# Performance work log

Measured on AMD Instinct MI355X. Metric: run time of the kernel, lower is better.

The kernel has to match this reference:

```python
import jax, jax.numpy as jnp
import numpy as np

B, DIM, H, W = 2, 128, 64, 64
DH, HEADS, K = 32, 4, 7  # dim_head, num_heads = dim // dim_head, kernel_size


def _ln(x, g, b):
    mu = jnp.mean(x, -1, keepdims=True)
    var = jnp.mean((x - mu) ** 2, -1, keepdims=True)
    return (x - mu) * jax.lax.rsqrt(var + 1e-5) * g + b


def _na2d(x, qkv_w, qkv_b, rpb, proj_w, proj_b):
    # NATTEN-style 2D neighborhood attention, dilation=1, edge-clamped windows.
    Bb, Hh, Ww, C = x.shape
    k = K
    qkv = (x @ qkv_w.T + qkv_b).reshape(Bb, Hh, Ww, 3, HEADS, DH).transpose(3, 0, 4, 1, 2, 5)
    q = qkv[0] * (DH ** -0.5)  # [B, heads, H, W, dh]
    kt, vt = qkv[1], qkv[2]
    def starts(n):
        return jnp.clip(jnp.arange(n) - k // 2, 0, n - k)
    nh = starts(Hh)[:, None] + jnp.arange(k)  # [H, k] absolute neighbor rows
    nw = starts(Ww)[:, None] + jnp.arange(k)  # [W, k] absolute neighbor cols
    ih = nh[:, None, :, None]  # [H,1,k,1]
    iw = nw[None, :, None, :]  # [1,W,1,k]
    Kw = kt[:, :, ih, iw, :]   # [B, heads, H, W, k, k, dh]
    Vw = vt[:, :, ih, iw, :]
    attn = jnp.einsum('bnhwd,bnhwijd->bnhwij', q, Kw)  # [B,heads,H,W,k,k]
    # relative positional bias, indices in [0, 2k-2]
    bih = (nh - jnp.arange(Hh)[:, None] + (k - 1))[:, None, :, None]
    biw = (nw - jnp.arange(Ww)[:, None] + (k - 1))[None, :, None, :]
    attn = attn + rpb[:, bih, biw][None]
    attn = jax.nn.softmax(attn.reshape(Bb, HEADS, Hh, Ww, k * k), -1).reshape(Bb, HEADS, Hh, Ww, k, k)
    out = jnp.einsum('bnhwij,bnhwijd->bnhwd', attn, Vw)
    out = out.transpose(0, 2, 3, 1, 4).reshape(Bb, Hh, Ww, C)
    return out @ proj_w.T + proj_b


def setup_inputs() -> dict:
    key = jax.random.key(0)
    ks = jax.random.split(key, 8)
    d = DIM
    w = lambda k_, sh: jax.random.normal(k_, sh, jnp.float32) * 0.02
    inp = {'x': jax.random.normal(ks[0], (B, DIM, H, W), jnp.float32)}
    inp.update(g1=jnp.ones(d), be1=jnp.zeros(d), g2=jnp.ones(d), be2=jnp.zeros(d),
               g3=jnp.ones(d), be3=jnp.zeros(d), g4=jnp.ones(d), be4=jnp.zeros(d))
    inp['qkv_w'] = w(ks[1], (3 * d, d)); inp['qkv_b'] = jnp.zeros(3 * d)
    inp['rpb'] = w(ks[2], (HEADS, 2 * K - 1, 2 * K - 1))
    inp['proj_w'] = w(ks[3], (d, d)); inp['proj_b'] = jnp.zeros(d)
    inp['w1'] = w(ks[4], (d, d)); inp['bl1'] = jnp.zeros(d)
    inp['w2'] = w(ks[5], (d, d)); inp['bl2'] = jnp.zeros(d)
    inp['w3'] = w(ks[6], (d, d)); inp['bl3'] = jnp.zeros(d)
    return inp


def reference(x, g1, be1, g2, be2, g3, be3, g4, be4, qkv_w, qkv_b, rpb, proj_w, proj_b, w1, bl1, w2, bl2, w3, bl3):
    x = x.transpose(0, 2, 3, 1)  # NCHW -> NHWC
    r = x
    y = _ln(x, g1, be1)
    y = _na2d(y, qkv_w, qkv_b, rpb, proj_w, proj_b)
    y = _ln(y, g2, be2)
    y = y @ w1.T + bl1
    x = y + r
    r = x
    y = _ln(x, g3, be3)
    y = y @ w2.T + bl2
    y = jax.nn.relu(y)
    y = _ln(y, g4, be4)
    y = y @ w3.T + bl3
    x = y + r
    return x.transpose(0, 3, 1, 2)  # NHWC -> NCHW
```

## Files before the change

kernel.cpp:

```cpp
#include <hip/hip_runtime.h>
#include <hip/hip_bf16.h>
#include <cstdint>

typedef short bf16x8 __attribute__((ext_vector_type(8)));
typedef float f32x4 __attribute__((ext_vector_type(4)));

#define NTOK 8192
#define QSCALE 0.17677669529663687f

__device__ inline float b2f(short s) {
  return __uint_as_float(((unsigned)(unsigned short)s) << 16);
}
__device__ inline short f2bs(float x) {
  __hip_bfloat16 b = __float2bfloat16(x);
  return *reinterpret_cast<short*>(&b);
}
__device__ inline bf16x8 ld8(const short* p) {
  short4 lo = *reinterpret_cast<const short4*>(p);
  short4 hi = *reinterpret_cast<const short4*>(p + 4);
  bf16x8 r;
  r[0] = lo.x; r[1] = lo.y; r[2] = lo.z; r[3] = lo.w;
  r[4] = hi.x; r[5] = hi.y; r[6] = hi.z; r[7] = hi.w;
  return r;
}

__global__ __launch_bounds__(256) void k_convw(
    const float* __restrict__ qw, const float* __restrict__ pw,
    const float* __restrict__ w1, const float* __restrict__ w2,
    const float* __restrict__ w3, __hip_bfloat16* __restrict__ dst) {
  int i = blockIdx.x * 256 + threadIdx.x;
  float v;
  if (i < 49152) v = qw[i];
  else if (i < 65536) v = pw[i - 49152];
  else if (i < 81920) v = w1[i - 65536];
  else if (i < 98304) v = w2[i - 81920];
  else if (i < 114688) v = w3[i - 98304];
  else return;
  dst[i] = __float2bfloat16(v);
}

__global__ __launch_bounds__(256) void k_qkvln(
    const float* __restrict__ x, const float* __restrict__ g,
    const float* __restrict__ be, const float* __restrict__ qkv_b,
    const __hip_bfloat16* __restrict__ wqkv, float* __restrict__ r,
    __hip_bfloat16* __restrict__ qkvb) {
  __shared__ float xt[128][33];
  __shared__ __hip_bfloat16 at[32][136];
  int t = threadIdx.x;
  int m0 = blockIdx.x * 32;
  int b = m0 >> 12;
  int p0 = m0 & 4095;
  const float* xb = x + (size_t)b * 524288;
  int tw = t & 31, th = t >> 5;
#pragma unroll
  for (int i = 0; i < 16; ++i) {
    int c = i * 8 + th;
    xt[c][tw] = xb[c * 4096 + p0 + tw];
  }
  __syncthreads();
  int wid = t >> 6, lane = t & 63;
  float gg0 = g[lane], gg1 = g[lane + 64];
  float bb0 = be[lane], bb1 = be[lane + 64];
#pragma unroll
  for (int it = 0; it < 8; ++it) {
    int tt = wid * 8 + it;
    float v0 = xt[lane][tt], v1 = xt[lane + 64][tt];
    float s = v0 + v1, sq = v0 * v0 + v1 * v1;
#pragma unroll
    for (int off = 32; off; off >>= 1) {
      s += __shfl_xor(s, off);
      sq += __shfl_xor(sq, off);
    }
    float mu = s * (1.f / 128.f);
    float var = sq * (1.f / 128.f) - mu * mu;
    float rs = rsqrtf(var + 1e-5f);
    r[(size_t)(m0 + tt) * 128 + lane] = v0;
    r[(size_t)(m0 + tt) * 128 + 64 + lane] = v1;
    at[tt][lane] = __float2bfloat16((v0 - mu) * rs * gg0 + bb0);
    at[tt][lane + 64] = __float2bfloat16((v1 - mu) * rs * gg1 + bb1);
  }
  __syncthreads();
  int mw = wid >> 1, nw = wid & 1;
  int lr = lane & 15, kg = lane >> 4;
  bf16x8 af[4];
#pragma unroll
  for (int ks = 0; ks < 4; ++ks)
    af[ks] = *reinterpret_cast<const bf16x8*>(&at[mw * 16 + lr][ks * 32 + kg * 8]);
  f32x4 acc[12];
#pragma unroll
  for (int nf = 0; nf < 12; ++nf) acc[nf] = f32x4{0, 0, 0, 0};
#pragma unroll
  for (int nf = 0; nf < 12; ++nf) {
    int o = nw * 192 + nf * 16 + lr;
    const __hip_bfloat16* wp = wqkv + o * 128 + kg * 8;
#pragma unroll
    for (int ks = 0; ks < 4; ++ks) {
      bf16x8 bfr = *reinterpret_cast<const bf16x8*>(wp + ks * 32);
      acc[nf] = __builtin_amdgcn_mfma_f32_16x16x32_bf16(af[ks], bfr, acc[nf], 0, 0, 0);
    }
  }
#pragma unroll
  for (int nf = 0; nf < 12; ++nf) {
    int o = nw * 192 + nf * 16 + lr;
    float bv = qkv_b[o];
    float qs = (o < 128) ? QSCALE : 1.f;
#pragma unroll
    for (int rr = 0; rr < 4; ++rr) {
      int m = m0 + mw * 16 + kg * 4 + rr;
      qkvb[(size_t)m * 384 + o] = __float2bfloat16((acc[nf][rr] + bv) * qs);
    }
  }
}

#define NB 98
#define KP 132
#define VP 108
#define PP 132
__global__ __launch_bounds__(256) void k_attn3(
    const __hip_bfloat16* __restrict__ qkv, const float* __restrict__ rpb,
    __hip_bfloat16* __restrict__ ao) {
  __shared__ __align__(16) short smem[104 * KP + 128 * VP + 4 * 8 * PP];
  short* Kl = smem;
  short* Vt = smem + 104 * KP;
  short* Pl = Vt + 128 * VP;
  const short* qs = (const short*)qkv;
  int tid = threadIdx.x;
  int m0 = blockIdx.x * 8;
  int b = m0 >> 12, hq = (m0 >> 6) & 63, c0 = m0 & 63;
  int hs = min(max(hq - 3, 0), 57);
  int cs0 = min(max(c0 - 3, 0), 50);
#pragma unroll
  for (int it = 0; it < 7; ++it) {
    int idx = it * 256 + tid;
    if (idx < NB * 16) {
      int row = idx >> 4, sub = idx & 15;
      int rh = row / 14, rc = row - rh * 14;
      int tr = b * 4096 + (hs + rh) * 64 + min(cs0 + rc, 63);
      const short* src = qs + (size_t)tr * 384 + 128 + sub * 8;
      *(short4*)(Kl + row * KP + sub * 8) = *(const short4*)src;
      *(short4*)(Kl + row * KP + sub * 8 + 4) = *(const short4*)(src + 4);
      const short* sv = qs + (size_t)tr * 384 + 256 + sub * 8;
      short4 vlo = *(const short4*)sv;
      short4 vhi = *(const short4*)(sv + 4);
      int d0 = sub * 8;
      Vt[(d0 + 0) * VP + row] = vlo.x;
      Vt[(d0 + 1) * VP + row] = vlo.y;
      Vt[(d0 + 2) * VP + row] = vlo.z;
      Vt[(d0 + 3) * VP + row] = vlo.w;
      Vt[(d0 + 4) * VP + row] = vhi.x;
      Vt[(d0 + 5) * VP + row] = vhi.y;
      Vt[(d0 + 6) * VP + row] = vhi.z;
      Vt[(d0 + 7) * VP + row] = vhi.w;
    }
  }
  {
    int row = tid >> 1, half = tid & 1;
#pragma unroll
    for (int e = 0; e < 5; ++e) Vt[row * VP + NB + half * 5 + e] = 0;
  }
  __syncthreads();
  int h = tid >> 6, lane = tid & 63;
  int lr = lane & 15, kg = lane >> 4;
  int qrow = min(m0 + lr, NTOK - 1);
  bf16x8 aq = *reinterpret_cast<const bf16x8*>(qs + (size_t)qrow * 384 + h * 32 + kg * 8);
  f32x4 sc[7];
#pragma unroll
  for (int nt = 0; nt < 7; ++nt) {
    bf16x8 bk = ld8(Kl + (nt * 16 + lr) * KP + h * 32 + kg * 8);
    sc[nt] = __builtin_amdgcn_mfma_f32_16x16x32_bf16(aq, bk, f32x4{0, 0, 0, 0}, 0, 0, 0);
  }
  int offv[4], cmt[4];
#pragma unroll
  for (int rr = 0; rr < 4; ++rr) {
    int ct = c0 + kg * 4 + rr;
    int ws0 = min(max(ct - 3, 0), 57);
    offv[rr] = ws0 - cs0;
    cmt[rr] = cs0 + 6 - ct;
  }
  float mx[4] = {-3e38f, -3e38f, -3e38f, -3e38f};
#pragma unroll
  for (int nt = 0; nt < 7; ++nt) {
    int nbr = nt * 16 + lr;
    int rh = nbr / 14, rc = nbr - rh * 14;
    bool vn = nbr < NB;
    int ribase = h * 169 + (hs - hq + 6 + rh) * 13 + rc;
#pragma unroll
    for (int rr = 0; rr < 4; ++rr) {
      float v = -1e30f;
      if (vn && (unsigned)(rc - offv[rr]) < 7u) v = sc[nt][rr] + rpb[ribase + cmt[rr]];
      sc[nt][rr] = v;
      mx[rr] = fmaxf(mx[rr], v);
    }
  }
#pragma unroll
  for (int rr = 0; rr < 4; ++rr) {
    mx[rr] = fmaxf(mx[rr], __shfl_xor(mx[rr], 1));
    mx[rr] = fmaxf(mx[rr], __shfl_xor(mx[rr], 2));
    mx[rr] = fmaxf(mx[rr], __shfl_xor(mx[rr], 4));
    mx[rr] = fmaxf(mx[rr], __shfl_xor(mx[rr], 8));
  }
  float sum[4] = {0.f, 0.f, 0.f, 0.f};
#pragma unroll
  for (int nt = 0; nt < 7; ++nt)
#pragma unroll
    for (int rr = 0; rr < 4; ++rr) {
      float e = __expf(sc[nt][rr] - mx[rr]);
      sc[nt][rr] = e;
      sum[rr] += e;
    }
#pragma unroll
  for (int rr = 0; rr < 4; ++rr) {
    sum[rr] += __shfl_xor(sum[rr], 1);
    sum[rr] += __shfl_xor(sum[rr], 2);
    sum[rr] += __shfl_xor(sum[rr], 4);
    sum[rr] += __shfl_xor(sum[rr], 8);
  }
  short* Ph = Pl + h * 8 * PP;
  if (kg < 2) {
#pragma unroll
    for (int rr = 0; rr < 4; ++rr) {
      float inv = 1.f / sum[rr];
      int tok = kg * 4 + rr;
#pragma unroll
      for (int nt = 0; nt < 7; ++nt)
        Ph[tok * PP + nt * 16 + lr] = f2bs(sc[nt][rr] * inv);
      Ph[tok * PP + 112 + lr] = 0;
      Ph[tok * PP + 128 + (lr & 3)] = 0;
    }
  }
  __syncthreads();
  f32x4 o[2] = {f32x4{0, 0, 0, 0}, f32x4{0, 0, 0, 0}};
#pragma unroll
  for (int kt = 0; kt < 4; ++kt) {
    bf16x8 ap = ld8(Ph + (lr & 7) * PP + kt * 32 + kg * 8);
#pragma unroll
    for (int dt = 0; dt < 2; ++dt) {
      bf16x8 bv = ld8(Vt + (h * 32 + dt * 16 + lr) * VP + kt * 32 + kg * 8);
      o[dt] = __builtin_amdgcn_mfma_f32_16x16x32_bf16(ap, bv, o[dt], 0, 0, 0);
    }
  }
  if (kg < 2) {
#pragma unroll
    for (int dt = 0; dt < 2; ++dt)
#pragma unroll
      for (int rr = 0; rr < 4; ++rr) {
        int tok = kg * 4 + rr;
        ao[(size_t)(m0 + tok) * 128 + h * 32 + dt * 16 + lr] =
            __float2bfloat16(o[dt][rr]);
      }
  }
}

template <bool A_GLOBAL>
__device__ inline void gemm_stage(const __hip_bfloat16* __restrict__ Aglob,
                                  const __hip_bfloat16 (*abuf)[136],
                                  const __hip_bfloat16* __restrict__ W,
                                  int mw, int nw, int lr, int kg, f32x4 acc[4]) {
  bf16x8 af[4];
  if constexpr (A_GLOBAL) {
#pragma unroll
    for (int ks = 0; ks < 4; ++ks)
      af[ks] = *reinterpret_cast<const bf16x8*>(Aglob + (mw * 16 + lr) * 128 + ks * 32 + kg * 8);
  } else {
#pragma unroll
    for (int ks = 0; ks < 4; ++ks)
      af[ks] = *reinterpret_cast<const bf16x8*>(&abuf[mw * 16 + lr][ks * 32 + kg * 8]);
  }
#pragma unroll
  for (int nf = 0; nf < 4; ++nf) {
    int o = nw * 64 + nf * 16 + lr;
    const __hip_bfloat16* wp = W + o * 128 + kg * 8;
    acc[nf] = f32x4{0, 0, 0, 0};
#pragma unroll
    for (int ks = 0; ks < 4; ++ks) {
      bf16x8 bfr = *reinterpret_cast<const bf16x8*>(wp + ks * 32);
      acc[nf] = __builtin_amdgcn_mfma_f32_16x16x32_bf16(af[ks], bfr, acc[nf], 0, 0, 0);
    }
  }
}

__device__ inline void ln_store(f32x4 acc[4], __hip_bfloat16 (*abuf)[136],
                                float2 (*red)[2][16],
                                const float* __restrict__ g,
                                const float* __restrict__ be,
                                int mw, int nw, int lr, int kg) {
  float ps[4] = {0.f, 0.f, 0.f, 0.f}, pq[4] = {0.f, 0.f, 0.f, 0.f};
#pragma unroll
  for (int nf = 0; nf < 4; ++nf)
#pragma unroll
    for (int rr = 0; rr < 4; ++rr) {
      float v = acc[nf][rr];
      ps[rr] += v;
      pq[rr] += v * v;
    }
#pragma unroll
  for (int rr = 0; rr < 4; ++rr)
#pragma unroll
    for (int off = 1; off < 16; off <<= 1) {
      ps[rr] += __shfl_xor(ps[rr], off);
      pq[rr] += __shfl_xor(pq[rr], off);
    }
  if (lr == 0)
#pragma unroll
    for (int rr = 0; rr < 4; ++rr)
      red[mw][nw][kg * 4 + rr] = make_float2(ps[rr], pq[rr]);
  __syncthreads();
  float mu[4], rs[4];
#pragma unroll
  for (int rr = 0; rr < 4; ++rr) {
    float2 a0 = red[mw][0][kg * 4 + rr], a1 = red[mw][1][kg * 4 + rr];
    mu[rr] = (a0.x + a1.x) * (1.f / 128.f);
    float var = (a0.y + a1.y) * (1.f / 128.f) - mu[rr] * mu[rr];
    rs[rr] = rsqrtf(var + 1e-5f);
  }
#pragma unroll
  for (int nf = 0; nf < 4; ++nf) {
    int o = nw * 64 + nf * 16 + lr;
    float gv = g[o], bev = be[o];
#pragma unroll
    for (int rr = 0; rr < 4; ++rr)
      abuf[mw * 16 + kg * 4 + rr][o] =
          __float2bfloat16((acc[nf][rr] - mu[rr]) * rs[rr] * gv + bev);
  }
}

__global__ __launch_bounds__(256) void k_tail(
    const __hip_bfloat16* __restrict__ ao, const float* __restrict__ r,
    const __hip_bfloat16* __restrict__ wproj, const float* __restrict__ bproj,
    const float* __restrict__ g2, const float* __restrict__ be2,
    const __hip_bfloat16* __restrict__ w1, const float* __restrict__ b1,
    const float* __restrict__ g3, const float* __restrict__ be3,
    const __hip_bfloat16* __restrict__ w2, const float* __restrict__ b2,
    const float* __restrict__ g4, const float* __restrict__ be4,
    const __hip_bfloat16* __restrict__ w3, const float* __restrict__ b3,
    float* __restrict__ out) {
  __shared__ __hip_bfloat16 abuf[32][136];
  __shared__ float2 red[2][2][16];
  int t = threadIdx.x, wid = t >> 6, lane = t & 63;
  int mw = wid >> 1, nw = wid & 1;
  int lr = lane & 15, kg = lane >> 4;
  int m0 = blockIdx.x * 32;
  f32x4 acc[4];
  float x2f[4][4];

  gemm_stage<true>(ao + (size_t)m0 * 128, nullptr, wproj, mw, nw, lr, kg, acc);
#pragma unroll
  for (int nf = 0; nf < 4; ++nf) {
    float bv = bproj[nw * 64 + nf * 16 + lr];
#pragma unroll
    for (int rr = 0; rr < 4; ++rr) acc[nf][rr] += bv;
  }
  ln_store(acc, abuf, red, g2, be2, mw, nw, lr, kg);
  __syncthreads();

  gemm_stage<false>(nullptr, abuf, w1, mw, nw, lr, kg, acc);
#pragma unroll
  for (int nf = 0; nf < 4; ++nf) {
    int o = nw * 64 + nf * 16 + lr;
    float bv = b1[o];
#pragma unroll
    for (int rr = 0; rr < 4; ++rr) {
      int m = m0 + mw * 16 + kg * 4 + rr;
      float v = acc[nf][rr] + bv + r[(size_t)m * 128 + o];
      x2f[nf][rr] = v;
      acc[nf][rr] = v;
    }
  }
  ln_store(acc, abuf, red, g3, be3, mw, nw, lr, kg);
  __syncthreads();

  gemm_stage<false>(nullptr, abuf, w2, mw, nw, lr, kg, acc);
#pragma unroll
  for (int nf = 0; nf < 4; ++nf) {
    float bv = b2[nw * 64 + nf * 16 + lr];
#pragma unroll
    for (int rr = 0; rr < 4; ++rr) acc[nf][rr] = fmaxf(acc[nf][rr] + bv, 0.f);
  }
  ln_store(acc, abuf, red, g4, be4, mw, nw, lr, kg);
  __syncthreads();

  gemm_stage<false>(nullptr, abuf, w3, mw, nw, lr, kg, acc);
#pragma unroll
  for (int nf = 0; nf < 4; ++nf) {
    int o = nw * 64 + nf * 16 + lr;
    float bv = b3[o];
#pragma unroll
    for (int rr = 0; rr < 4; ++rr) {
      int m = m0 + mw * 16 + kg * 4 + rr;
      float v = acc[nf][rr] + bv + x2f[nf][rr];
      int bb = m >> 12, hw = m & 4095;
      out[(size_t)bb * 524288 + o * 4096 + hw] = v;
    }
  }
}

extern "C" void kernel_launch(void* const* d_in, const int* in_sizes, int n_in,
                              void* d_out, int out_size, void* d_ws,
                              size_t ws_size, hipStream_t stream) {
  const float* x = (const float*)d_in[0];
  const float* g1 = (const float*)d_in[1];
  const float* be1 = (const float*)d_in[2];
  const float* g2 = (const float*)d_in[3];
  const float* be2 = (const float*)d_in[4];
  const float* g3 = (const float*)d_in[5];
  const float* be3 = (const float*)d_in[6];
  const float* g4 = (const float*)d_in[7];
  const float* be4 = (const float*)d_in[8];
  const float* qkv_w = (const float*)d_in[9];
  const float* qkv_b = (const float*)d_in[10];
  const float* rpb = (const float*)d_in[11];
  const float* proj_w = (const float*)d_in[12];
  const float* proj_b = (const float*)d_in[13];
  const float* w1 = (const float*)d_in[14];
  const float* bl1 = (const float*)d_in[15];
  const float* w2 = (const float*)d_in[16];
  const float* bl2 = (const float*)d_in[17];
  const float* w3 = (const float*)d_in[18];
  const float* bl3 = (const float*)d_in[19];

  char* ws = (char*)d_ws;
  __hip_bfloat16* wb = (__hip_bfloat16*)ws;
  __hip_bfloat16* wb_qkv = wb;
  __hip_bfloat16* wb_proj = wb + 49152;
  __hip_bfloat16* wb_w1 = wb + 65536;
  __hip_bfloat16* wb_w2 = wb + 81920;
  __hip_bfloat16* wb_w3 = wb + 98304;
  float* r = (float*)(ws + 262144);
  __hip_bfloat16* qkvb = (__hip_bfloat16*)(ws + 4456448);
  __hip_bfloat16* ao = (__hip_bfloat16*)(ws + 10747904);

  k_convw<<<448, 256, 0, stream>>>(qkv_w, proj_w, w1, w2, w3, wb);
  k_qkvln<<<256, 256, 0, stream>>>(x, g1, be1, qkv_b, wb_qkv, r, qkvb);
  k_attn3<<<1024, 256, 0, stream>>>(qkvb, rpb, ao);
  k_tail<<<256, 256, 0, stream>>>(ao, r, wb_proj, proj_b, g2, be2, wb_w1, bl1,
                                  g3, be3, wb_w2, bl2, g4, be4, wb_w3, bl3,
                                  (float*)d_out);
}
```

Before: 56.12 us.

## Fuse attention with MLP tail and fold weight conversion into QKV kernel

Merges the weight-conversion kernel into the QKV/LayerNorm kernel, which now converts QKV weights to bf16 in registers and has each block convert a slice of the remaining weights. The attention kernel and the projection/MLP tail are fused so each block computes attention for 32 tokens in four 8-token passes and keeps the result in LDS. This removes two launches and the global round-trip of the attention output. In exchange, the attention phase runs on a quarter as many blocks with serialized passes, which reduces parallelism and latency hiding.

After: 63.38 us. +12.9%, slower.

```diff
diff --git a/kernel.cpp b/kernel.cpp
--- a/kernel.cpp
+++ b/kernel.cpp
@@ -23,30 +23,32 @@
   r[4] = hi.x; r[5] = hi.y; r[6] = hi.z; r[7] = hi.w;
   return r;
 }
-
-__global__ __launch_bounds__(256) void k_convw(
-    const float* __restrict__ qw, const float* __restrict__ pw,
-    const float* __restrict__ w1, const float* __restrict__ w2,
-    const float* __restrict__ w3, __hip_bfloat16* __restrict__ dst) {
-  int i = blockIdx.x * 256 + threadIdx.x;
-  float v;
-  if (i < 49152) v = qw[i];
-  else if (i < 65536) v = pw[i - 49152];
-  else if (i < 81920) v = w1[i - 65536];
-  else if (i < 98304) v = w2[i - 81920];
-  else if (i < 114688) v = w3[i - 98304];
-  else return;
-  dst[i] = __float2bfloat16(v);
-}
-
-__global__ __launch_bounds__(256) void k_qkvln(
+__device__ inline bf16x8 cvt8(float4 a, float4 c) {
+  bf16x8 r;
+  r[0] = f2bs(a.x); r[1] = f2bs(a.y); r[2] = f2bs(a.z); r[3] = f2bs(a.w);
+  r[4] = f2bs(c.x); r[5] = f2bs(c.y); r[6] = f2bs(c.z); r[7] = f2bs(c.w);
+  return r;
+}
+
+__global__ __launch_bounds__(256) void k_qkvcw(
     const float* __restrict__ x, const float* __restrict__ g,
     const float* __restrict__ be, const float* __restrict__ qkv_b,
-    const __hip_bfloat16* __restrict__ wqkv, float* __restrict__ r,
-    __hip_bfloat16* __restrict__ qkvb) {
+    const float* __restrict__ qkv_w, const float* __restrict__ pw,
+    const float* __restrict__ w1f, const float* __restrict__ w2f,
+    const float* __restrict__ w3f, __hip_bfloat16* __restrict__ wb,
+    float* __restrict__ r, __hip_bfloat16* __restrict__ qkvb) {
   __shared__ float xt[128][33];
   __shared__ __hip_bfloat16 at[32][136];
   int t = threadIdx.x;
+  {
+    int ci = blockIdx.x * 256 + t;
+    float cv;
+    if (ci < 16384) cv = pw[ci];
+    else if (ci < 32768) cv = w1f[ci - 16384];
+    else if (ci < 49152) cv = w2f[ci - 32768];
+    else cv = w3f[ci - 49152];
+    wb[ci] = __float2bfloat16(cv);
+  }
   int m0 = blockIdx.x * 32;
   int b = m0 >> 12;
   int p0 = m0 & 4095;
@@ -92,11 +94,13 @@
 #pragma unroll
   for (int nf = 0; nf < 12; ++nf) {
     int o = nw * 192 + nf * 16 + lr;
-    const __hip_bfloat16* wp = wqkv + o * 128 + kg * 8;
+    const float* wp = qkv_w + o * 128 + kg * 8;
 #pragma unroll
     for (int ks = 0; ks < 4; ++ks) {
-      bf16x8 bfr = *reinterpret_cast<const bf16x8*>(wp + ks * 32);
-      acc[nf] = __builtin_amdgcn_mfma_f32_16x16x32_bf16(af[ks], bfr, acc[nf], 0, 0, 0);
+      float4 wa = *reinterpret_cast<const float4*>(wp + ks * 32);
+      float4 wc = *reinterpret_cast<const float4*>(wp + ks * 32 + 4);
+      acc[nf] = __builtin_amdgcn_mfma_f32_16x16x32_bf16(af[ks], cvt8(wa, wc),
+                                                        acc[nf], 0, 0, 0);
     }
   }
 #pragma unroll
@@ -116,244 +120,235 @@
 #define KP 132
 #define VP 108
 #define PP 132
-__global__ __launch_bounds__(256) void k_attn3(
-    const __hip_bfloat16* __restrict__ qkv, const float* __restrict__ rpb,
-    __hip_bfloat16* __restrict__ ao) {
+__global__ __launch_bounds__(256) void k_fuse2(
+    const __hip_bfloat16* __restrict__ qkvb, const float* __restrict__ rpb,
+    const float* __restrict__ r, const __hip_bfloat16* __restrict__ wb,
+    const float* __restrict__ bproj,
+    const float* __restrict__ g2, const float* __restrict__ be2,
+    const float* __restrict__ b1,
+    const float* __restrict__ g3, const float* __restrict__ be3,
+    const float* __restrict__ b2,
+    const float* __restrict__ g4, const float* __restrict__ be4,
+    const float* __restrict__ b3, float* __restrict__ out) {
   __shared__ __align__(16) short smem[104 * KP + 128 * VP + 4 * 8 * PP];
+  __shared__ __align__(16) __hip_bfloat16 abuf[32][136];
+  __shared__ float2 red[2][2][16];
   short* Kl = smem;
   short* Vt = smem + 104 * KP;
   short* Pl = Vt + 128 * VP;
-  const short* qs = (const short*)qkv;
+  const short* qs = (const short*)qkvb;
   int tid = threadIdx.x;
-  int m0 = blockIdx.x * 8;
-  int b = m0 >> 12, hq = (m0 >> 6) & 63, c0 = m0 & 63;
+  int m0 = blockIdx.x * 32;
+  int b = m0 >> 12, hq = (m0 >> 6) & 63;
   int hs = min(max(hq - 3, 0), 57);
-  int cs0 = min(max(c0 - 3, 0), 50);
-#pragma unroll
-  for (int it = 0; it < 7; ++it) {
-    int idx = it * 256 + tid;
-    if (idx < NB * 16) {
-      int row = idx >> 4, sub = idx & 15;
-      int rh = row / 14, rc = row - rh * 14;
-      int tr = b * 4096 + (hs + rh) * 64 + min(cs0 + rc, 63);
-      const short* src = qs + (size_t)tr * 384 + 128 + sub * 8;
-      *(short4*)(Kl + row * KP + sub * 8) = *(const short4*)src;
-      *(short4*)(Kl + row * KP + sub * 8 + 4) = *(const short4*)(src + 4);
-      const short* sv = qs + (size_t)tr * 384 + 256 + sub * 8;
-      short4 vlo = *(const short4*)sv;
-      short4 vhi = *(const short4*)(sv + 4);
-      int d0 = sub * 8;
-      Vt[(d0 + 0) * VP + row] = vlo.x;
-      Vt[(d0 + 1) * VP + row] = vlo.y;
-      Vt[(d0 + 2) * VP + row] = vlo.z;
-      Vt[(d0 + 3) * VP + row] = vlo.w;
-      Vt[(d0 + 4) * VP + row] = vhi.x;
-      Vt[(d0 + 5) * VP + row] = vhi.y;
-      Vt[(d0 + 6) * VP + row] = vhi.z;
-      Vt[(d0 + 7) * VP + row] = vhi.w;
-    }
-  }
-  {
-    int row = tid >> 1, half = tid & 1;
-#pragma unroll
-    for (int e = 0; e < 5; ++e) Vt[row * VP + NB + half * 5 + e] = 0;
-  }
-  __syncthreads();
   int h = tid >> 6, lane = tid & 63;
   int lr = lane & 15, kg = lane >> 4;
-  int qrow = min(m0 + lr, NTOK - 1);
-  bf16x8 aq = *reinterpret_cast<const bf16x8*>(qs + (size_t)qrow * 384 + h * 32 + kg * 8);
-  f32x4 sc[7];
-#pragma unroll
-  for (int nt = 0; nt < 7; ++nt) {
-    bf16x8 bk = ld8(Kl + (nt * 16 + lr) * KP + h * 32 + kg * 8);
-    sc[nt] = __builtin_amdgcn_mfma_f32_16x16x32_bf16(aq, bk, f32x4{0, 0, 0, 0}, 0, 0, 0);
-  }
-  int offv[4], cmt[4];
-#pragma unroll
-  for (int rr = 0; rr < 4; ++rr) {
-    int ct = c0 + kg * 4 + rr;
-    int ws0 = min(max(ct - 3, 0), 57);
-    offv[rr] = ws0 - cs0;
-    cmt[rr] = cs0 + 6 - ct;
-  }
-  float mx[4] = {-3e38f, -3e38f, -3e38f, -3e38f};
-#pragma unroll
-  for (int nt = 0; nt < 7; ++nt) {
-    int nbr = nt * 16 + lr;
-    int rh = nbr / 14, rc = nbr - rh * 14;
-    bool vn = nbr < NB;
-    int ribase = h * 169 + (hs - hq + 6 + rh) * 13 + rc;
-#pragma unroll
-    for (int rr = 0; rr < 4; ++rr) {
-      float v = -1e30f;
-      if (vn && (unsigned)(rc - offv[rr]) < 7u) v = sc[nt][rr] + rpb[ribase + cmt[rr]];
-      sc[nt][rr] = v;
-      mx[rr] = fmaxf(mx[rr], v);
-    }
-  }
-#pragma unroll
-  for (int rr = 0; rr < 4; ++rr) {
-    mx[rr] = fmaxf(mx[rr], __shfl_xor(mx[rr], 1));
-    mx[rr] = fmaxf(mx[rr], __shfl_xor(mx[rr], 2));
-    mx[rr] = fmaxf(mx[rr], __shfl_xor(mx[rr], 4));
-    mx[rr] = fmaxf(mx[rr], __shfl_xor(mx[rr], 8));
-  }
-  float sum[4] = {0.f, 0.f, 0.f, 0.f};
-#pragma unroll
-  for (int nt = 0; nt < 7; ++nt)
-#pragma unroll
-    for (int rr = 0; rr < 4; ++rr) {
-      float e = __expf(sc[nt][rr] - mx[rr]);
-      sc[nt][rr] = e;
-      sum[rr] += e;
-    }
-#pragma unroll
-  for (int rr = 0; rr < 4; ++rr) {
-    sum[rr] += __shfl_xor(sum[rr], 1);
-    sum[rr] += __shfl_xor(sum[rr], 2);
-    sum[rr] += __shfl_xor(sum[rr], 4);
-    sum[rr] += __shfl_xor(sum[rr], 8);
-  }
-  short* Ph = Pl + h * 8 * PP;
-  if (kg < 2) {
-#pragma unroll
-    for (int rr = 0; rr < 4; ++rr) {
-      float inv = 1.f / sum[rr];
-      int tok = kg * 4 + rr;
-#pragma unroll
-      for (int nt = 0; nt < 7; ++nt)
-        Ph[tok * PP + nt * 16 + lr] = f2bs(sc[nt][rr] * inv);
-      Ph[tok * PP + 112 + lr] = 0;
-      Ph[tok * PP + 128 + (lr & 3)] = 0;
-    }
-  }
-  __syncthreads();
-  f32x4 o[2] = {f32x4{0, 0, 0, 0}, f32x4{0, 0, 0, 0}};
-#pragma unroll
-  for (int kt = 0; kt < 4; ++kt) {
-    bf16x8 ap = ld8(Ph + (lr & 7) * PP + kt * 32 + kg * 8);
-#pragma unroll
-    for (int dt = 0; dt < 2; ++dt) {
-      bf16x8 bv = ld8(Vt + (h * 32 + dt * 16 + lr) * VP + kt * 32 + kg * 8);
-      o[dt] = __builtin_amdgcn_mfma_f32_16x16x32_bf16(ap, bv, o[dt], 0, 0, 0);
-    }
-  }
-  if (kg < 2) {
-#pragma unroll
-    for (int dt = 0; dt < 2; ++dt)
+  const __hip_bfloat16* wproj = wb;
+  const __hip_bfloat16* w1 = wb + 16384;
+  const __hip_bfloat16* w2 = wb + 32768;
+  const __hip_bfloat16* w3 = wb + 49152;
+
+  {
+    int rowz = tid >> 1, halfz = tid & 1;
+#pragma unroll
+    for (int e = 0; e < 5; ++e) Vt[rowz * VP + NB + halfz * 5 + e] = 0;
+  }
+
+  for (int s = 0; s < 4; ++s) {
+    __syncthreads();
+    int ms = m0 + s * 8;
+    int c0s = (m0 & 63) + s * 8;
+    int cs0 = min(max(c0s - 3, 0), 50);
+#pragma unroll
+    for (int it = 0; it < 7; ++it) {
+      int idx = it * 256 + tid;
+      if (idx < NB * 16) {
+        int row = idx >> 4, sub = idx & 15;
+        int rh = row / 14, rc = row - rh * 14;
+        int tr = b * 4096 + (hs + rh) * 64 + min(cs0 + rc, 63);
+        const short* src = qs + (size_t)tr * 384 + 128 + sub * 8;
+        *(short4*)(Kl + row * KP + sub * 8) = *(const short4*)src;
+        *(short4*)(Kl + row * KP + sub * 8 + 4) = *(const short4*)(src + 4);
+        const short* sv = qs + (size_t)tr * 384 + 256 + sub * 8;
+        short4 vlo = *(const short4*)sv;
+        short4 vhi = *(const short4*)(sv + 4);
+        int d0 = sub * 8;
+        Vt[(d0 + 0) * VP + row] = vlo.x;
+        Vt[(d0 + 1) * VP + row] = vlo.y;
+        Vt[(d0 + 2) * VP + row] = vlo.z;
+        Vt[(d0 + 3) * VP + row] = vlo.w;
+        Vt[(d0 + 4) * VP + row] = vhi.x;
+        Vt[(d0 + 5) * VP + row] = vhi.y;
+        Vt[(d0 + 6) * VP + row] = vhi.z;
+        Vt[(d0 + 7) * VP + row] = vhi.w;
+      }
+    }
+    __syncthreads();
+    int qrow = min(ms + lr, NTOK - 1);
+    bf16x8 aq = *reinterpret_cast<const bf16x8*>(qs + (size_t)qrow * 384 + h * 32 + kg * 8);
+    f32x4 sc[7];
+#pragma unroll
+    for (int nt = 0; nt < 7; ++nt) {
+      bf16x8 bk = ld8(Kl + (nt * 16 + lr) * KP + h * 32 + kg * 8);
+      sc[nt] = __builtin_amdgcn_mfma_f32_16x16x32_bf16(aq, bk, f32x4{0, 0, 0, 0}, 0, 0, 0);
+    }
+    int offv[4], cmt[4];
+#pragma unroll
+    for (int rr = 0; rr < 4; ++rr) {
+      int ct = c0s + kg * 4 + rr;
+      int ws0 = min(max(ct - 3, 0), 57);
+      offv[rr] = ws0 - cs0;
+      cmt[rr] = cs0 + 6 - ct;
+    }
+    float mx[4] = {-3e38f, -3e38f, -3e38f, -3e38f};
+#pragma unroll
+    for (int nt = 0; nt < 7; ++nt) {
+      int nbr = nt * 16 + lr;
+      int rh = nbr / 14, rc = nbr - rh * 14;
+      bool vn = nbr < NB;
+      int ribase = h * 169 + (hs - hq + 6 + rh) * 13 + rc;
 #pragma unroll
       for (int rr = 0; rr < 4; ++rr) {
+        float v = -1e30f;
+        if (vn && (unsigned)(rc - offv[rr]) < 7u) v = sc[nt][rr] + rpb[ribase + cmt[rr]];
+        sc[nt][rr] = v;
+        mx[rr] = fmaxf(mx[rr], v);
+      }
+    }
+#pragma unroll
+    for (int rr = 0; rr < 4; ++rr) {
+      mx[rr] = fmaxf(mx[rr], __shfl_xor(mx[rr], 1));
+      mx[rr] = fmaxf(mx[rr], __shfl_xor(mx[rr], 2));
+      mx[rr] = fmaxf(mx[rr], __shfl_xor(mx[rr], 4));
+      mx[rr] = fmaxf(mx[rr], __shfl_xor(mx[rr], 8));
+    }
+    float sum[4] = {0.f, 0.f, 0.f, 0.f};
+#pragma unroll
+    for (int nt = 0; nt < 7; ++nt)
+#pragma unroll
+      for (int rr = 0; rr < 4; ++rr) {
+        float e = __expf(sc[nt][rr] - mx[rr]);
+        sc[nt][rr] = e;
+        sum[rr] += e;
+      }
+#pragma unroll
+    for (int rr = 0; rr < 4; ++rr) {
+      sum[rr] += __shfl_xor(sum[rr], 1);
+      sum[rr] += __shfl_xor(sum[rr], 2);
+      sum[rr] += __shfl_xor(sum[rr], 4);
+      sum[rr] += __shfl_xor(sum[rr], 8);
+    }
+    short* Ph = Pl + h * 8 * PP;
+    if (kg < 2) {
+#pragma unroll
+      for (int rr = 0; rr < 4; ++rr) {
+        float inv = 1.f / sum[rr];
         int tok = kg * 4 + rr;
-        ao[(size_t)(m0 + tok) * 128 + h * 32 + dt * 16 + lr] =
-            __float2bfloat16(o[dt][rr]);
-      }
-  }
-}
-
-template <bool A_GLOBAL>
-__device__ inline void gemm_stage(const __hip_bfloat16* __restrict__ Aglob,
-                                  const __hip_bfloat16 (*abuf)[136],
-                                  const __hip_bfloat16* __restrict__ W,
-                                  int mw, int nw, int lr, int kg, f32x4 acc[4]) {
-  bf16x8 af[4];
-  if constexpr (A_GLOBAL) {
-#pragma unroll
-    for (int ks = 0; ks < 4; ++ks)
-      af[ks] = *reinterpret_cast<const bf16x8*>(Aglob + (mw * 16 + lr) * 128 + ks * 32 + kg * 8);
-  } else {
+#pragma unroll
+        for (int nt = 0; nt < 7; ++nt)
+          Ph[tok * PP + nt * 16 + lr] = f2bs(sc[nt][rr] * inv);
+        Ph[tok * PP + 112 + lr] = 0;
+        Ph[tok * PP + 128 + (lr & 3)] = 0;
+      }
+    }
+    __syncthreads();
+    f32x4 o2[2] = {f32x4{0, 0, 0, 0}, f32x4{0, 0, 0, 0}};
+#pragma unroll
+    for (int kt = 0; kt < 4; ++kt) {
+      bf16x8 ap = ld8(Ph + (lr & 7) * PP + kt * 32 + kg * 8);
+#pragma unroll
+      for (int dt = 0; dt < 2; ++dt) {
+        bf16x8 bv = ld8(Vt + (h * 32 + dt * 16 + lr) * VP + kt * 32 + kg * 8);
+        o2[dt] = __builtin_amdgcn_mfma_f32_16x16x32_bf16(ap, bv, o2[dt], 0, 0, 0);
+      }
+    }
+    if (kg < 2) {
+#pragma unroll
+      for (int dt = 0; dt < 2; ++dt)
+#pragma unroll
+        for (int rr = 0; rr < 4; ++rr)
+          abuf[s * 8 + kg * 4 + rr][h * 32 + dt * 16 + lr] =
+              __float2bfloat16(o2[dt][rr]);
+    }
+  }
+  __syncthreads();
+
+  int wid = tid >> 6;
+  int mw = wid >> 1, nw = wid & 1;
+  f32x4 acc[4];
+  float x2f[4][4];
+
+  auto gemm_lds = [&](const __hip_bfloat16* W) {
+    bf16x8 af[4];
 #pragma unroll
     for (int ks = 0; ks < 4; ++ks)
       af[ks] = *reinterpret_cast<const bf16x8*>(&abuf[mw * 16 + lr][ks * 32 + kg * 8]);
-  }
-#pragma unroll
-  for (int nf = 0; nf < 4; ++nf) {
-    int o = nw * 64 + nf * 16 + lr;
-    const __hip_bfloat16* wp = W + o * 128 + kg * 8;
-    acc[nf] = f32x4{0, 0, 0, 0};
-#pragma unroll
-    for (int ks = 0; ks < 4; ++ks) {
-      bf16x8 bfr = *reinterpret_cast<const bf16x8*>(wp + ks * 32);
-      acc[nf] = __builtin_amdgcn_mfma_f32_16x16x32_bf16(af[ks], bfr, acc[nf], 0, 0, 0);
-    }
-  }
-}
-
-__device__ inline void ln_store(f32x4 acc[4], __hip_bfloat16 (*abuf)[136],
-                                float2 (*red)[2][16],
-                                const float* __restrict__ g,
-                                const float* __restrict__ be,
-                                int mw, int nw, int lr, int kg) {
-  float ps[4] = {0.f, 0.f, 0.f, 0.f}, pq[4] = {0.f, 0.f, 0.f, 0.f};
-#pragma unroll
-  for (int nf = 0; nf < 4; ++nf)
-#pragma unroll
-    for (int rr = 0; rr < 4; ++rr) {
-      float v = acc[nf][rr];
-      ps[rr] += v;
-      pq[rr] += v * v;
-    }
-#pragma unroll
-  for (int rr = 0; rr < 4; ++rr)
-#pragma unroll
-    for (int off = 1; off < 16; off <<= 1) {
-      ps[rr] += __shfl_xor(ps[rr], off);
-      pq[rr] += __shfl_xor(pq[rr], off);
-    }
-  if (lr == 0)
+#pragma unroll
+    for (int nf = 0; nf < 4; ++nf) {
+      int o = nw * 64 + nf * 16 + lr;
+      const __hip_bfloat16* wp = W + o * 128 + kg * 8;
+      acc[nf] = f32x4{0, 0, 0, 0};
+#pragma unroll
+      for (int ks = 0; ks < 4; ++ks) {
+        bf16x8 bfr = *reinterpret_cast<const bf16x8*>(wp + ks * 32);
+        acc[nf] = __builtin_amdgcn_mfma_f32_16x16x32_bf16(af[ks], bfr, acc[nf], 0, 0, 0);
+      }
+    }
+  };
+  auto ln_store = [&](const float* g, const float* be) {
+    float ps[4] = {0.f, 0.f, 0.f, 0.f}, pq[4] = {0.f, 0.f, 0.f, 0.f};
+#pragma unroll
+    for (int nf = 0; nf < 4; ++nf)
+#pragma unroll
+      for (int rr = 0; rr < 4; ++rr) {
+        float v = acc[nf][rr];
+        ps[rr] += v;
+        pq[rr] += v * v;
+      }
 #pragma unroll
     for (int rr = 0; rr < 4; ++rr)
-      red[mw][nw][kg * 4 + rr] = make_float2(ps[rr], pq[rr]);
-  __syncthreads();
-  float mu[4], rs[4];
-#pragma unroll
-  for (int rr = 0; rr < 4; ++rr) {
-    float2 a0 = red[mw][0][kg * 4 + rr], a1 = red[mw][1][kg * 4 + rr];
-    mu[rr] = (a0.x + a1.x) * (1.f / 128.f);
-    float var = (a0.y + a1.y) * (1.f / 128.f) - mu[rr] * mu[rr];
-    rs[rr] = rsqrtf(var + 1e-5f);
-  }
-#pragma unroll
-  for (int nf = 0; nf < 4; ++nf) {
-    int o = nw * 64 + nf * 16 + lr;
-    float gv = g[o], bev = be[o];
-#pragma unroll
-    for (int rr = 0; rr < 4; ++rr)
-      abuf[mw * 16 + kg * 4 + rr][o] =
-          __float2bfloat16((acc[nf][rr] - mu[rr]) * rs[rr] * gv + bev);
-  }
-}
-
-__global__ __launch_bounds__(256) void k_tail(
-    const __hip_bfloat16* __restrict__ ao, const float* __restrict__ r,
-    const __hip_bfloat16* __restrict__ wproj, const float* __restrict__ bproj,
-    const float* __restrict__ g2, const float* __restrict__ be2,
-    const __hip_bfloat16* __restrict__ w1, const float* __restrict__ b1,
-    const float* __restrict__ g3, const float* __restrict__ be3,
-    const __hip_bfloat16* __restrict__ w2, const float* __restrict__ b2,
-    const float* __restrict__ g4, const float* __restrict__ be4,
-    const __hip_bfloat16* __restrict__ w3, const float* __restrict__ b3,
-    float* __restrict__ out) {
-  __shared__ __hip_bfloat16 abuf[32][136];
-  __shared__ float2 red[2][2][16];
-  int t = threadIdx.x, wid = t >> 6, lane = t & 63;
-  int mw = wid >> 1, nw = wid & 1;
-  int lr = lane & 15, kg = lane >> 4;
-  int m0 = blockIdx.x * 32;
-  f32x4 acc[4];
-  float x2f[4][4];
-
-  gemm_stage<true>(ao + (size_t)m0 * 128, nullptr, wproj, mw, nw, lr, kg, acc);
+#pragma unroll
+      for (int off = 1; off < 16; off <<= 1) {
+        ps[rr] += __shfl_xor(ps[rr], off);
+        pq[rr] += __shfl_xor(pq[rr], off);
+      }
+    if (lr == 0)
+#pragma unroll
+      for (int rr = 0; rr < 4; ++rr)
+        red[mw][nw][kg * 4 + rr] = make_float2(ps[rr], pq[rr]);
+    __syncthreads();
+    float mu[4], rs[4];
+#pragma unroll
+    for (int rr = 0; rr < 4; ++rr) {
+      float2 a0 = red[mw][0][kg * 4 + rr], a1 = red[mw][1][kg * 4 + rr];
+      mu[rr] = (a0.x + a1.x) * (1.f / 128.f);
+      float var = (a0.y + a1.y) * (1.f / 128.f) - mu[rr] * mu[rr];
+      rs[rr] = rsqrtf(var + 1e-5f);
+    }
+#pragma unroll
+    for (int nf = 0; nf < 4; ++nf) {
+      int o = nw * 64 + nf * 16 + lr;
+      float gv = g[o], bev = be[o];
+#pragma unroll
+      for (int rr = 0; rr < 4; ++rr)
+        abuf[mw * 16 + kg * 4 + rr][o] =
+            __float2bfloat16((acc[nf][rr] - mu[rr]) * rs[rr] * gv + bev);
+    }
+    __syncthreads();
+  };
+
+  gemm_lds(wproj);
+  __syncthreads();
 #pragma unroll
   for (int nf = 0; nf < 4; ++nf) {
     float bv = bproj[nw * 64 + nf * 16 + lr];
 #pragma unroll
     for (int rr = 0; rr < 4; ++rr) acc[nf][rr] += bv;
   }
-  ln_store(acc, abuf, red, g2, be2, mw, nw, lr, kg);
-  __syncthreads();
-
-  gemm_stage<false>(nullptr, abuf, w1, mw, nw, lr, kg, acc);
+  ln_store(g2, be2);
+
+  gemm_lds(w1);
+  __syncthreads();
 #pragma unroll
   for (int nf = 0; nf < 4; ++nf) {
     int o = nw * 64 + nf * 16 + lr;
@@ -366,20 +361,19 @@
       acc[nf][rr] = v;
     }
   }
-  ln_store(acc, abuf, red, g3, be3, mw, nw, lr, kg);
-  __syncthreads();
-
-  gemm_stage<false>(nullptr, abuf, w2, mw, nw, lr, kg, acc);
+  ln_store(g3, be3);
+
+  gemm_lds(w2);
+  __syncthreads();
 #pragma unroll
   for (int nf = 0; nf < 4; ++nf) {
     float bv = b2[nw * 64 + nf * 16 + lr];
 #pragma unroll
     for (int rr = 0; rr < 4; ++rr) acc[nf][rr] = fmaxf(acc[nf][rr] + bv, 0.f);
   }
-  ln_store(acc, abuf, red, g4, be4, mw, nw, lr, kg);
-  __syncthreads();
-
-  gemm_stage<false>(nullptr, abuf, w3, mw, nw, lr, kg, acc);
+  ln_store(g4, be4);
+
+  gemm_lds(w3);
 #pragma unroll
   for (int nf = 0; nf < 4; ++nf) {
     int o = nw * 64 + nf * 16 + lr;
@@ -420,19 +414,11 @@
 
   char* ws = (char*)d_ws;
   __hip_bfloat16* wb = (__hip_bfloat16*)ws;
-  __hip_bfloat16* wb_qkv = wb;
-  __hip_bfloat16* wb_proj = wb + 49152;
-  __hip_bfloat16* wb_w1 = wb + 65536;
-  __hip_bfloat16* wb_w2 = wb + 81920;
-  __hip_bfloat16* wb_w3 = wb + 98304;
   float* r = (float*)(ws + 262144);
   __hip_bfloat16* qkvb = (__hip_bfloat16*)(ws + 4456448);
-  __hip_bfloat16* ao = (__hip_bfloat16*)(ws + 10747904);
-
-  k_convw<<<448, 256, 0, stream>>>(qkv_w, proj_w, w1, w2, w3, wb);
-  k_qkvln<<<256, 256, 0, stream>>>(x, g1, be1, qkv_b, wb_qkv, r, qkvb);
-  k_attn3<<<1024, 256, 0, stream>>>(qkvb, rpb, ao);
-  k_tail<<<256, 256, 0, stream>>>(ao, r, wb_proj, proj_b, g2, be2, wb_w1, bl1,
-                                  g3, be3, wb_w2, bl2, g4, be4, wb_w3, bl3,
-                                  (float*)d_out);
-}
+
+  k_qkvcw<<<256, 256, 0, stream>>>(x, g1, be1, qkv_b, qkv_w, proj_w, w1, w2,
+                                   w3, wb, r, qkvb);
+  k_fuse2<<<256, 256, 0, stream>>>(qkvb, rpb, r, wb, proj_b, g2, be2, bl1, g3,
+                                   be3, bl2, g4, be4, bl3, (float*)d_out);
+}
```
